# Kernel optimization log

Measured on AMD Instinct MI355X. Metric: run time of the kernel, lower is better.

Reference implementation:

```python
import jax, jax.numpy as jnp
import numpy as np

H = 64  # GRU hidden size


def _gru_scan(x_proj, m, U, b_rec):
    # x_proj: [S,B,3H] precomputed input projections (time-major); m: [S,B] bool mask
    B = x_proj.shape[1]
    h0 = jnp.zeros((B, H), x_proj.dtype)

    def step(h, inp):
        xp, mt = inp
        rec = h @ U + b_rec                       # [B,3H] (Keras reset_after=True)
        xz, xr, xh = jnp.split(xp, 3, axis=-1)
        rz, rr, rh = jnp.split(rec, 3, axis=-1)
        z = jax.nn.sigmoid(xz + rz)
        r = jax.nn.sigmoid(xr + rr)
        hh = jnp.tanh(xh + r * rh)
        hn = z * h + (1.0 - z) * hh
        hn = jnp.where(mt[:, None], hn, h)        # masked steps carry state through
        return hn, hn

    hT, hs = jax.lax.scan(step, h0, (x_proj, m))
    return hs, hT  # hs: [S,B,H], hT: [B,H]


def setup_inputs() -> dict:
    key = jax.random.key(0)
    ks = jax.random.split(key, 16)
    V, E = 50000, 25
    B, S, T = 512, 200, 10
    s = 0.05
    f32 = jnp.float32
    inp = {
        "input_batch": jax.random.randint(ks[0], (B, S, T), 0, V),
        "emb_table": jax.random.normal(ks[1], (V, E), f32) * s,
        "W_f": jax.random.normal(ks[2], (E, 3 * H), f32) * s,
        "U_f": jax.random.normal(ks[3], (H, 3 * H), f32) * s,
        "b_f": jnp.zeros((2, 3 * H), f32),
        "W_b": jax.random.normal(ks[4], (E, 3 * H), f32) * s,
        "U_b": jax.random.normal(ks[5], (H, 3 * H), f32) * s,
        "b_b": jnp.zeros((2, 3 * H), f32),
        "W_k": jax.random.normal(ks[6], (2 * H, H), f32) * s,
        "b_k": jnp.zeros((H,), f32),
        "W_q": jax.random.normal(ks[7], (H, H), f32) * s,
        "b_q": jnp.zeros((H,), f32),
        "W_e": jax.random.normal(ks[8], (H, 1), f32) * s,
        "b_e": jnp.zeros((1,), f32),
    }
    return inp


def reference(input_batch, emb_table, W_f, U_f, b_f, W_b, U_b, b_b, W_k, b_k, W_q, b_q, W_e, b_e):
    mask = input_batch != 0                                  # [B,S,T]
    emb = emb_table[input_batch]                             # [B,S,T,E]
    nm = mask.astype(emb.dtype)
    denom = nm.sum(axis=2)                                   # [B,S]
    denom = jnp.where(denom == 0, jnp.ones_like(denom), denom)
    x = (emb * nm[..., None]).sum(axis=2) / denom[..., None] # [B,S,E] masked mean over tags
    step_mask = mask[:, :, 0]                                # [B,S] GRU step mask

    xT = jnp.swapaxes(x, 0, 1)                               # [S,B,E]
    mT = jnp.swapaxes(step_mask, 0, 1)                       # [S,B]

    # forward GRU
    hs_f, hT_f = _gru_scan(xT @ W_f + b_f[0], mT, U_f, b_f[1])
    # backward GRU: reverse time, scan, reverse back
    hs_b, _ = _gru_scan((xT @ W_b + b_b[0])[::-1], mT[::-1], U_b, b_b[1])
    hs_b = hs_b[::-1]

    out = jnp.swapaxes(jnp.concatenate([hs_f, hs_b], axis=-1), 0, 1)  # [B,S,2H]

    # Bahdanau attention; query = forward final state
    keys = out @ W_k + b_k                                   # [B,S,H]
    queries = hT_f @ W_q + b_q                               # [B,H]
    e = jnp.tanh(keys + queries[:, None, :]) @ W_e + b_e     # [B,S,1]
    e = e + (1.0 - step_mask.astype(e.dtype))[..., None] * -1e9
    w = jax.nn.softmax(e, axis=1)                            # [B,S,1]
    context = (w * out).sum(axis=1)                          # [B,2H]
    return context
```

## Files before the change

### kernel.cpp

```cpp
#include <hip/hip_runtime.h>
#include <math.h>

#define BATCH 512
#define SEQ   200
#define TOK   10
#define EMB   25
#define HID   64
#define G3    192

__device__ __forceinline__ float fast_sigmoid(float t) {
    float e = __expf(-t);
    return __builtin_amdgcn_rcpf(1.f + e);
}
__device__ __forceinline__ float fast_tanh(float t) {
    float e2 = __expf(2.f * t);
    return 1.f - 2.f * __builtin_amdgcn_rcpf(e2 + 1.f);
}

__global__ __launch_bounds__(256) void emb_mean_kernel(
    const int* __restrict__ ids_g, const float* __restrict__ emb,
    float* __restrict__ x, float* __restrict__ mask)
{
    int grp  = blockIdx.x * 8 + (threadIdx.x >> 5);
    int lane = threadIdx.x & 31;
    if (grp >= BATCH * SEQ) return;
    const int* ids = ids_g + (size_t)grp * TOK;
    float acc = 0.f;
    int cnt = 0;
    #pragma unroll
    for (int t = 0; t < TOK; t++) {
        int id = ids[t];
        if (id != 0) {
            cnt++;
            if (lane < EMB) acc += emb[(size_t)id * EMB + lane];
        }
    }
    if (lane < EMB)
        x[(size_t)grp * EMB + lane] = cnt ? acc / (float)cnt : 0.f;
    if (lane == 0)
        mask[grp] = (ids[0] != 0) ? 1.f : 0.f;
}

__global__ __launch_bounds__(64, 1) void gru_kernel(
    const float* __restrict__ xg, const float* __restrict__ maskg,
    const float* __restrict__ W_f, const float* __restrict__ U_f, const float* __restrict__ b_f,
    const float* __restrict__ W_b, const float* __restrict__ U_b, const float* __restrict__ b_b,
    float* __restrict__ outg, float* __restrict__ hT)
{
    const int bidx = blockIdx.x;
    const int dir  = bidx >> 9;
    const int b    = bidx & 511;
    const int j    = threadIdx.x;

    const float* W    = dir ? W_b : W_f;
    const float* U    = dir ? U_b : U_f;
    const float* bias = dir ? b_b : b_f;

    float Uz[HID], Ur[HID], Uh[HID];
    #pragma unroll
    for (int k = 0; k < HID; k++) {
        Uz[k] = U[k * G3 + j];
        Ur[k] = U[k * G3 + HID + j];
        Uh[k] = U[k * G3 + 2 * HID + j];
    }
    float Wz[EMB], Wr[EMB], Wh[EMB];
    #pragma unroll
    for (int e = 0; e < EMB; e++) {
        Wz[e] = W[e * G3 + j];
        Wr[e] = W[e * G3 + HID + j];
        Wh[e] = W[e * G3 + 2 * HID + j];
    }
    const float bz0 = bias[j];
    const float br0 = bias[HID + j];
    const float bh0 = bias[2 * HID + j];
    const float bzr = bias[G3 + j];
    const float brr = bias[G3 + HID + j];
    const float bhr = bias[G3 + 2 * HID + j];

    __shared__ float xs[SEQ * EMB];
    __shared__ float ms[SEQ];
    __shared__ float hs[HID];

    {
        const float4* xrow4 = (const float4*)(xg + (size_t)b * (SEQ * EMB));
        float4* xs4 = (float4*)xs;
        for (int i = j; i < (SEQ * EMB) / 4; i += 64) xs4[i] = xrow4[i];
        for (int i = j; i < SEQ; i += 64) ms[i] = maskg[(size_t)b * SEQ + i];
        hs[j] = 0.f;
    }
    __syncthreads();

    float h = 0.f;
    float* orow_base = outg + (size_t)b * SEQ * (2 * HID) + dir * HID + j;

    for (int step = 0; step < SEQ; step++) {
        const int s = dir ? (SEQ - 1 - step) : step;

        const float* xr = xs + s * EMB;
        float pz = bz0, pr = br0, ph = bh0;
        #pragma unroll
        for (int e = 0; e < EMB; e++) {
            float xv = xr[e];
            pz = fmaf(xv, Wz[e], pz);
            pr = fmaf(xv, Wr[e], pr);
            ph = fmaf(xv, Wh[e], ph);
        }

        float az = bzr, ar = brr, ah = bhr;
        #pragma unroll
        for (int k = 0; k < HID; k++) {
            float hk = hs[k];
            az = fmaf(hk, Uz[k], az);
            ar = fmaf(hk, Ur[k], ar);
            ah = fmaf(hk, Uh[k], ah);
        }

        float z  = fast_sigmoid(pz + az);
        float r  = fast_sigmoid(pr + ar);
        float hh = fast_tanh(ph + r * ah);
        float hn = z * h + (1.f - z) * hh;
        hn = (ms[s] != 0.f) ? hn : h;
        h = hn;

        __builtin_amdgcn_wave_barrier();
        hs[j] = hn;
        __builtin_amdgcn_wave_barrier();

        orow_base[(size_t)s * (2 * HID)] = hn;
    }
    if (dir == 0) hT[(size_t)b * HID + j] = h;
}

__global__ __launch_bounds__(256) void attn_kernel(
    const float* __restrict__ outg, const float* __restrict__ maskg,
    const float* __restrict__ hT,
    const float* __restrict__ W_k, const float* __restrict__ b_k,
    const float* __restrict__ W_q, const float* __restrict__ b_q,
    const float* __restrict__ W_e, const float* __restrict__ b_e,
    float* __restrict__ ctx)
{
    const int b   = blockIdx.x;
    const int tid = threadIdx.x;

    __shared__ float Wks[2 * HID * HID];
    __shared__ float qs[HID];
    __shared__ float es[SEQ];

    for (int i = tid; i < 2 * HID * HID; i += 256) Wks[i] = W_k[i];
    if (tid < HID) {
        float q = b_q[tid];
        const float* hrow = hT + (size_t)b * HID;
        #pragma unroll 8
        for (int i = 0; i < HID; i++) q = fmaf(hrow[i], W_q[i * HID + tid], q);
        qs[tid] = q;
    }
    __syncthreads();

    const int wave = tid >> 6;
    const int lane = tid & 63;
    const float bk = b_k[lane];
    const float we = W_e[lane];
    const float be = b_e[0];

    for (int s = wave; s < SEQ; s += 4) {
        const float* orow = outg + ((size_t)b * SEQ + s) * (2 * HID);
        float a0 = 0.f, a1 = 0.f, a2 = 0.f, a3 = 0.f;
        #pragma unroll
        for (int i = 0; i < 2 * HID; i += 4) {
            a0 = fmaf(orow[i + 0], Wks[(i + 0) * HID + lane], a0);
            a1 = fmaf(orow[i + 1], Wks[(i + 1) * HID + lane], a1);
            a2 = fmaf(orow[i + 2], Wks[(i + 2) * HID + lane], a2);
            a3 = fmaf(orow[i + 3], Wks[(i + 3) * HID + lane], a3);
        }
        float t = tanhf(((a0 + a1) + (a2 + a3)) + bk + qs[lane]) * we;
        #pragma unroll
        for (int off = 32; off > 0; off >>= 1) t += __shfl_down(t, off);
        if (lane == 0) {
            float pen = (maskg[(size_t)b * SEQ + s] != 0.f) ? 0.f : -1e9f;
            es[s] = t + be + pen;
        }
    }
    __syncthreads();

    if (tid < 64) {
        float mx = -1e30f;
        for (int s2 = tid; s2 < SEQ; s2 += 64) mx = fmaxf(mx, es[s2]);
        #pragma unroll
        for (int off = 32; off > 0; off >>= 1) mx = fmaxf(mx, __shfl_xor(mx, off));
        float sum = 0.f;
        for (int s2 = tid; s2 < SEQ; s2 += 64) {
            float w = expf(es[s2] - mx);
            es[s2] = w;
            sum += w;
        }
        #pragma unroll
        for (int off = 32; off > 0; off >>= 1) sum += __shfl_xor(sum, off);
        float inv = 1.f / sum;
        for (int s2 = tid; s2 < SEQ; s2 += 64) es[s2] *= inv;
    }
    __syncthreads();

    if (tid < 2 * HID) {
        const int jj = tid;
        float a0 = 0.f, a1 = 0.f;
        for (int s2 = 0; s2 < SEQ; s2 += 2) {
            a0 = fmaf(es[s2],     outg[((size_t)b * SEQ + s2)     * (2 * HID) + jj], a0);
            a1 = fmaf(es[s2 + 1], outg[((size_t)b * SEQ + s2 + 1) * (2 * HID) + jj], a1);
        }
        ctx[(size_t)b * (2 * HID) + jj] = a0 + a1;
    }
}

extern "C" void kernel_launch(void* const* d_in, const int* in_sizes, int n_in,
                              void* d_out, int out_size, void* d_ws, size_t ws_size,
                              hipStream_t stream) {
    const int*   ids = (const int*)  d_in[0];
    const float* emb = (const float*)d_in[1];
    const float* W_f = (const float*)d_in[2];
    const float* U_f = (const float*)d_in[3];
    const float* b_f = (const float*)d_in[4];
    const float* W_b = (const float*)d_in[5];
    const float* U_b = (const float*)d_in[6];
    const float* b_b = (const float*)d_in[7];
    const float* W_k = (const float*)d_in[8];
    const float* b_k = (const float*)d_in[9];
    const float* W_q = (const float*)d_in[10];
    const float* b_q = (const float*)d_in[11];
    const float* W_e = (const float*)d_in[12];
    const float* b_e = (const float*)d_in[13];

    float* ws   = (float*)d_ws;
    float* x    = ws;
    float* mask = ws + 2560000;
    float* out  = ws + 2662400;
    float* hT   = ws + 15769600;

    emb_mean_kernel<<<(BATCH * SEQ) / 8, 256, 0, stream>>>(ids, emb, x, mask);
    gru_kernel<<<1024, 64, 0, stream>>>(x, mask, W_f, U_f, b_f,
                                        W_b, U_b, b_b, out, hT);
    attn_kernel<<<BATCH, 256, 0, stream>>>(out, mask, hT, W_k, b_k,
                                           W_q, b_q, W_e, b_e, (float*)d_out);
}
```

Baseline: 466.3 us.

## Precompute GRU input projections in embedding kernel and prefetch them in recurrence

The embedding-mean kernel now also computes the forward and backward input projections (x@W + b) for every position and writes a 384-wide row per position. The GRU kernel then only does the recurrent matvec, using float4 LDS reads of h and split accumulators, and software-prefetches projected inputs two steps ahead. The attention kernel gets float4 row loads and splits the context reduction across all 256 threads. This takes the input projection off the serial critical path, at the cost of roughly 157 MB of extra global traffic for the xp buffer.

```diff
diff --git a/kernel.cpp b/kernel.cpp
--- a/kernel.cpp
+++ b/kernel.cpp
@@ -7,6 +7,7 @@
 #define EMB   25
 #define HID   64
 #define G3    192
+#define XPW   384
 
 __device__ __forceinline__ float fast_sigmoid(float t) {
     float e = __expf(-t);
@@ -17,34 +18,66 @@
     return 1.f - 2.f * __builtin_amdgcn_rcpf(e2 + 1.f);
 }
 
-__global__ __launch_bounds__(256) void emb_mean_kernel(
+__global__ __launch_bounds__(256, 2) void emb_xproj_kernel(
     const int* __restrict__ ids_g, const float* __restrict__ emb,
-    float* __restrict__ x, float* __restrict__ mask)
+    const float* __restrict__ W_f, const float* __restrict__ b_f,
+    const float* __restrict__ W_b, const float* __restrict__ b_b,
+    float* __restrict__ xp, float* __restrict__ mask)
 {
-    int grp  = blockIdx.x * 8 + (threadIdx.x >> 5);
-    int lane = threadIdx.x & 31;
-    if (grp >= BATCH * SEQ) return;
-    const int* ids = ids_g + (size_t)grp * TOK;
-    float acc = 0.f;
-    int cnt = 0;
+    const int lane = threadIdx.x & 63;
+    const int wave = threadIdx.x >> 6;
+
+    float Wreg[EMB][6];
+    float bl[6];
     #pragma unroll
-    for (int t = 0; t < TOK; t++) {
-        int id = ids[t];
-        if (id != 0) {
-            cnt++;
-            if (lane < EMB) acc += emb[(size_t)id * EMB + lane];
-        }
-    }
-    if (lane < EMB)
-        x[(size_t)grp * EMB + lane] = cnt ? acc / (float)cnt : 0.f;
-    if (lane == 0)
-        mask[grp] = (ids[0] != 0) ? 1.f : 0.f;
+    for (int g = 0; g < 3; g++) {
+        #pragma unroll
+        for (int e = 0; e < EMB; e++) {
+            Wreg[e][g]     = W_f[e * G3 + g * 64 + lane];
+            Wreg[e][g + 3] = W_b[e * G3 + g * 64 + lane];
+        }
+        bl[g]     = b_f[g * 64 + lane];
+        bl[g + 3] = b_b[g * 64 + lane];
+    }
+
+    for (int pos = blockIdx.x * 4 + wave; pos < BATCH * SEQ; pos += gridDim.x * 4) {
+        const int* ids = ids_g + (size_t)pos * TOK;
+        float acc = 0.f;
+        int cnt = 0;
+        #pragma unroll
+        for (int t = 0; t < TOK; t++) {
+            int id = ids[t];
+            if (id != 0) {
+                cnt++;
+                if (lane < EMB) acc += emb[(size_t)id * EMB + lane];
+            }
+        }
+        float xv = cnt ? acc / (float)cnt : 0.f;
+        if (lane == 0) mask[pos] = (ids[0] != 0) ? 1.f : 0.f;
+
+        float xr[EMB];
+        #pragma unroll
+        for (int e = 0; e < EMB; e++) xr[e] = __shfl(xv, e);
+
+        float* orow = xp + (size_t)pos * XPW;
+        #pragma unroll
+        for (int g = 0; g < 6; g++) {
+            float a0 = bl[g], a1 = 0.f;
+            #pragma unroll
+            for (int e = 0; e < 24; e += 2) {
+                a0 = fmaf(xr[e + 0], Wreg[e + 0][g], a0);
+                a1 = fmaf(xr[e + 1], Wreg[e + 1][g], a1);
+            }
+            a0 = fmaf(xr[24], Wreg[24][g], a0);
+            orow[g * 64 + lane] = a0 + a1;
+        }
+    }
 }
 
 __global__ __launch_bounds__(64, 1) void gru_kernel(
-    const float* __restrict__ xg, const float* __restrict__ maskg,
-    const float* __restrict__ W_f, const float* __restrict__ U_f, const float* __restrict__ b_f,
-    const float* __restrict__ W_b, const float* __restrict__ U_b, const float* __restrict__ b_b,
+    const float* __restrict__ xp, const float* __restrict__ maskg,
+    const float* __restrict__ U_f, const float* __restrict__ b_f,
+    const float* __restrict__ U_b, const float* __restrict__ b_b,
     float* __restrict__ outg, float* __restrict__ hT)
 {
     const int bidx = blockIdx.x;
@@ -52,7 +85,6 @@
     const int b    = bidx & 511;
     const int j    = threadIdx.x;
 
-    const float* W    = dir ? W_b : W_f;
     const float* U    = dir ? U_b : U_f;
     const float* bias = dir ? b_b : b_f;
 
@@ -63,61 +95,53 @@
         Ur[k] = U[k * G3 + HID + j];
         Uh[k] = U[k * G3 + 2 * HID + j];
     }
-    float Wz[EMB], Wr[EMB], Wh[EMB];
-    #pragma unroll
-    for (int e = 0; e < EMB; e++) {
-        Wz[e] = W[e * G3 + j];
-        Wr[e] = W[e * G3 + HID + j];
-        Wh[e] = W[e * G3 + 2 * HID + j];
-    }
-    const float bz0 = bias[j];
-    const float br0 = bias[HID + j];
-    const float bh0 = bias[2 * HID + j];
     const float bzr = bias[G3 + j];
     const float brr = bias[G3 + HID + j];
     const float bhr = bias[G3 + 2 * HID + j];
 
-    __shared__ float xs[SEQ * EMB];
     __shared__ float ms[SEQ];
-    __shared__ float hs[HID];
-
-    {
-        const float4* xrow4 = (const float4*)(xg + (size_t)b * (SEQ * EMB));
-        float4* xs4 = (float4*)xs;
-        for (int i = j; i < (SEQ * EMB) / 4; i += 64) xs4[i] = xrow4[i];
-        for (int i = j; i < SEQ; i += 64) ms[i] = maskg[(size_t)b * SEQ + i];
-        hs[j] = 0.f;
-    }
-    __syncthreads();
+    __shared__ __align__(16) float hs[HID];
+
+    for (int i = j; i < SEQ; i += 64) ms[i] = maskg[(size_t)b * SEQ + i];
+    hs[j] = 0.f;
+    __syncthreads();
+
+    const float* xpb = xp + (size_t)b * SEQ * XPW + dir * G3 + j;
+    float* orow_base = outg + (size_t)b * SEQ * (2 * HID) + dir * HID + j;
+    const float4* hs4 = (const float4*)hs;
+
+    int s = dir ? (SEQ - 1) : 0;
+    const int st = dir ? -1 : 1;
+
+    size_t o0 = (size_t)s * XPW;
+    float cz = xpb[o0], cr = xpb[o0 + 64], ch = xpb[o0 + 128];
+    size_t o1 = (size_t)(s + st) * XPW;
+    float nz = xpb[o1], nr = xpb[o1 + 64], nh = xpb[o1 + 128];
 
     float h = 0.f;
-    float* orow_base = outg + (size_t)b * SEQ * (2 * HID) + dir * HID + j;
-
-    for (int step = 0; step < SEQ; step++) {
-        const int s = dir ? (SEQ - 1 - step) : step;
-
-        const float* xr = xs + s * EMB;
-        float pz = bz0, pr = br0, ph = bh0;
-        #pragma unroll
-        for (int e = 0; e < EMB; e++) {
-            float xv = xr[e];
-            pz = fmaf(xv, Wz[e], pz);
-            pr = fmaf(xv, Wr[e], pr);
-            ph = fmaf(xv, Wh[e], ph);
-        }
-
-        float az = bzr, ar = brr, ah = bhr;
-        #pragma unroll
-        for (int k = 0; k < HID; k++) {
-            float hk = hs[k];
-            az = fmaf(hk, Uz[k], az);
-            ar = fmaf(hk, Ur[k], ar);
-            ah = fmaf(hk, Uh[k], ah);
-        }
-
-        float z  = fast_sigmoid(pz + az);
-        float r  = fast_sigmoid(pr + ar);
-        float hh = fast_tanh(ph + r * ah);
+    for (int step = 0; step < SEQ; step++, s += st) {
+        float tz = 0.f, tr = 0.f, th = 0.f;
+        if (step + 2 < SEQ) {
+            size_t o2 = (size_t)(s + 2 * st) * XPW;
+            tz = xpb[o2]; tr = xpb[o2 + 64]; th = xpb[o2 + 128];
+        }
+
+        float az0 = bzr, az1 = 0.f, ar0 = brr, ar1 = 0.f, ah0 = bhr, ah1 = 0.f;
+        #pragma unroll
+        for (int k4 = 0; k4 < HID / 4; k4++) {
+            float4 hv = hs4[k4];
+            int k = k4 * 4;
+            az0 = fmaf(hv.x, Uz[k],     az0); az1 = fmaf(hv.y, Uz[k + 1], az1);
+            az0 = fmaf(hv.z, Uz[k + 2], az0); az1 = fmaf(hv.w, Uz[k + 3], az1);
+            ar0 = fmaf(hv.x, Ur[k],     ar0); ar1 = fmaf(hv.y, Ur[k + 1], ar1);
+            ar0 = fmaf(hv.z, Ur[k + 2], ar0); ar1 = fmaf(hv.w, Ur[k + 3], ar1);
+            ah0 = fmaf(hv.x, Uh[k],     ah0); ah1 = fmaf(hv.y, Uh[k + 1], ah1);
+            ah0 = fmaf(hv.z, Uh[k + 2], ah0); ah1 = fmaf(hv.w, Uh[k + 3], ah1);
+        }
+
+        float z  = fast_sigmoid(cz + az0 + az1);
+        float r  = fast_sigmoid(cr + ar0 + ar1);
+        float hh = fast_tanh(ch + r * (ah0 + ah1));
         float hn = z * h + (1.f - z) * hh;
         hn = (ms[s] != 0.f) ? hn : h;
         h = hn;
@@ -127,6 +151,9 @@
         __builtin_amdgcn_wave_barrier();
 
         orow_base[(size_t)s * (2 * HID)] = hn;
+
+        cz = nz; cr = nr; ch = nh;
+        nz = tz; nr = tr; nh = th;
     }
     if (dir == 0) hT[(size_t)b * HID + j] = h;
 }
@@ -145,6 +172,7 @@
     __shared__ float Wks[2 * HID * HID];
     __shared__ float qs[HID];
     __shared__ float es[SEQ];
+    __shared__ float part[2 * HID];
 
     for (int i = tid; i < 2 * HID * HID; i += 256) Wks[i] = W_k[i];
     if (tid < HID) {
@@ -163,14 +191,16 @@
     const float be = b_e[0];
 
     for (int s = wave; s < SEQ; s += 4) {
-        const float* orow = outg + ((size_t)b * SEQ + s) * (2 * HID);
+        const float4* orow4 = (const float4*)(outg + ((size_t)b * SEQ + s) * (2 * HID));
         float a0 = 0.f, a1 = 0.f, a2 = 0.f, a3 = 0.f;
         #pragma unroll
-        for (int i = 0; i < 2 * HID; i += 4) {
-            a0 = fmaf(orow[i + 0], Wks[(i + 0) * HID + lane], a0);
-            a1 = fmaf(orow[i + 1], Wks[(i + 1) * HID + lane], a1);
-            a2 = fmaf(orow[i + 2], Wks[(i + 2) * HID + lane], a2);
-            a3 = fmaf(orow[i + 3], Wks[(i + 3) * HID + lane], a3);
+        for (int i4 = 0; i4 < (2 * HID) / 4; i4++) {
+            float4 ov = orow4[i4];
+            int i = i4 * 4;
+            a0 = fmaf(ov.x, Wks[(i + 0) * HID + lane], a0);
+            a1 = fmaf(ov.y, Wks[(i + 1) * HID + lane], a1);
+            a2 = fmaf(ov.z, Wks[(i + 2) * HID + lane], a2);
+            a3 = fmaf(ov.w, Wks[(i + 3) * HID + lane], a3);
         }
         float t = tanhf(((a0 + a1) + (a2 + a3)) + bk + qs[lane]) * we;
         #pragma unroll
@@ -200,14 +230,16 @@
     }
     __syncthreads();
 
-    if (tid < 2 * HID) {
-        const int jj = tid;
-        float a0 = 0.f, a1 = 0.f;
-        for (int s2 = 0; s2 < SEQ; s2 += 2) {
-            a0 = fmaf(es[s2],     outg[((size_t)b * SEQ + s2)     * (2 * HID) + jj], a0);
-            a1 = fmaf(es[s2 + 1], outg[((size_t)b * SEQ + s2 + 1) * (2 * HID) + jj], a1);
-        }
-        ctx[(size_t)b * (2 * HID) + jj] = a0 + a1;
+    {
+        const int half = tid >> 7;
+        const int jj   = tid & 127;
+        float a = 0.f;
+        for (int s2 = half; s2 < SEQ; s2 += 2)
+            a = fmaf(es[s2], outg[((size_t)b * SEQ + s2) * (2 * HID) + jj], a);
+        if (half == 1) part[jj] = a;
+        __syncthreads();
+        if (half == 0)
+            ctx[(size_t)b * (2 * HID) + jj] = a + part[jj];
     }
 }
 
@@ -230,14 +262,14 @@
     const float* b_e = (const float*)d_in[13];
 
     float* ws   = (float*)d_ws;
-    float* x    = ws;
-    float* mask = ws + 2560000;
-    float* out  = ws + 2662400;
-    float* hT   = ws + 15769600;
-
-    emb_mean_kernel<<<(BATCH * SEQ) / 8, 256, 0, stream>>>(ids, emb, x, mask);
-    gru_kernel<<<1024, 64, 0, stream>>>(x, mask, W_f, U_f, b_f,
-                                        W_b, U_b, b_b, out, hT);
+    float* xp   = ws;
+    float* mask = ws + 39321600;
+    float* out  = ws + 39424000;
+    float* hT   = ws + 52531200;
+
+    emb_xproj_kernel<<<1280, 256, 0, stream>>>(ids, emb, W_f, b_f, W_b, b_b,
+                                               xp, mask);
+    gru_kernel<<<1024, 64, 0, stream>>>(xp, mask, U_f, b_f, U_b, b_b, out, hT);
     attn_kernel<<<BATCH, 256, 0, stream>>>(out, mask, hT, W_k, b_k,
                                            W_q, b_q, W_e, b_e, (float*)d_out);
 }
```

Result: slower. 640.0 us (+37.3%).
